# Kernel optimization log

Measured on AMD Instinct MI355X. Metric: run time of the kernel, lower is better.

The kernel has to match this reference:

```python
import jax, jax.numpy as jnp
import numpy as np

EPS = 1e-08
LAM = 0.01


def setup_inputs() -> dict:
    key = jax.random.key(0)
    k1, k2, k3 = jax.random.split(key, 3)
    BS, L, N = 256, 2048, 128
    pred_weights = jax.random.normal(k1, (BS, L, N), dtype=jnp.float32)
    # positive prices in [0.5, 1.5) to avoid div-by-zero / inf
    price_list = jax.random.uniform(k2, (BS, L + 1, N), dtype=jnp.float32, minval=0.5, maxval=1.5)
    # valid lengths in [2, L] (torch.var is unbiased -> need n >= 2)
    pred_sz = jax.random.randint(k3, (BS, 1), 2, L + 1, dtype=jnp.int64)
    return {"pred_weights": pred_weights, "price_list": price_list, "pred_sz": pred_sz}


def reference(pred_weights, price_list, pred_sz):
    P_i = price_list[:, :-1, :]  # [BS, L, N] past prices
    P_j = price_list[:, 1:, :]   # [BS, L, N] future prices
    r = jnp.nan_to_num((P_j - P_i) / P_i)
    r = r * (r <= 2)             # zero out returns > 2 (outlier mask)

    L = r.shape[1]
    Rp = jnp.sum(pred_weights[:, :L, :] * r, axis=-1)  # [BS, L] portfolio returns

    n = pred_sz.reshape(-1).astype(Rp.dtype)                       # [BS]
    mask = (jnp.arange(L)[None, :] < pred_sz.reshape(-1, 1)).astype(Rp.dtype)  # [BS, L]

    expected_Rp = jnp.sum(Rp * mask, axis=1) / n                   # masked mean
    centered = (Rp - expected_Rp[:, None]) * mask
    variance_Rp = jnp.sum(centered * centered, axis=1) / (n - 1)   # unbiased var (torch.var default)

    denom = jnp.sqrt(variance_Rp + EPS)
    sharpe = expected_Rp / denom
    sharpe_list = expected_Rp - LAM / denom

    return (-jnp.mean(sharpe_list), -jnp.mean(sharpe), jnp.mean(expected_Rp), jnp.mean(variance_Rp))
```

## Files before the change

### kernel.cpp

```cpp
#include <hip/hip_runtime.h>

#define EPS 1e-8f
#define LAM 0.01f

constexpr int BS = 256;
constexpr int L  = 2048;
constexpr int N  = 128;
constexpr int CHUNK  = 128;
constexpr int NCHUNK = L / CHUNK;


__global__ __launch_bounds__(256) void rp_kernel(
    const float* __restrict__ w,
    const float* __restrict__ price,
    const int*  __restrict__ pred_sz,
    float* __restrict__ ws)
{
    const int b     = blockIdx.x / NCHUNK;
    const int chunk = blockIdx.x % NCHUNK;
    const int n     = pred_sz[b];

    const int start = chunk * CHUNK;
    if (start >= n) return;
    const int end = min(start + CHUNK, n);

    const int tid  = threadIdx.x;
    const int grp  = tid >> 5;
    const int lane = tid & 31;

    float s1 = 0.0f, s2 = 0.0f;

    const int l0 = start + grp;
    const float* wp = w     + ((size_t)b * L       + l0) * N + lane * 4;
    const float* pp = price + ((size_t)b * (L + 1) + l0) * N + lane * 4;

    #pragma unroll 4
    for (int l = l0; l < end; l += 8, wp += 8 * N, pp += 8 * N) {
        const float4 wv = *reinterpret_cast<const float4*>(wp);
        const float4 pi = *reinterpret_cast<const float4*>(pp);
        const float4 pj = *reinterpret_cast<const float4*>(pp + N);

        float r0 = (pj.x - pi.x) * __builtin_amdgcn_rcpf(pi.x);
        float r1 = (pj.y - pi.y) * __builtin_amdgcn_rcpf(pi.y);
        float r2 = (pj.z - pi.z) * __builtin_amdgcn_rcpf(pi.z);
        float r3 = (pj.w - pi.w) * __builtin_amdgcn_rcpf(pi.w);
        r0 = (r0 <= 2.0f) ? r0 : 0.0f;
        r1 = (r1 <= 2.0f) ? r1 : 0.0f;
        r2 = (r2 <= 2.0f) ? r2 : 0.0f;
        r3 = (r3 <= 2.0f) ? r3 : 0.0f;

        float acc = wv.x * r0 + wv.y * r1 + wv.z * r2 + wv.w * r3;

        #pragma unroll
        for (int m = 1; m < 32; m <<= 1)
            acc += __shfl_xor(acc, m);

        if (lane == 0) {
            s1 += acc;
            s2 += acc * acc;
        }
    }

    __shared__ float ls1[8], ls2[8];
    if (lane == 0) { ls1[grp] = s1; ls2[grp] = s2; }
    __syncthreads();
    if (tid == 0) {
        float t1 = 0.0f, t2 = 0.0f;
        #pragma unroll
        for (int i = 0; i < 8; ++i) { t1 += ls1[i]; t2 += ls2[i]; }
        ws[b * NCHUNK + chunk]              = t1;
        ws[BS * NCHUNK + b * NCHUNK + chunk] = t2;
    }
}

__global__ __launch_bounds__(256) void final_kernel(
    const float* __restrict__ ws,
    const int*  __restrict__ pred_sz,
    float* __restrict__ out)
{
    const int b = threadIdx.x;
    const int ni = pred_sz[b];
    const int nc = (ni + CHUNK - 1) / CHUNK;

    float s1 = 0.0f, s2 = 0.0f;
    for (int c = 0; c < nc; ++c) {
        s1 += ws[b * NCHUNK + c];
        s2 += ws[BS * NCHUNK + b * NCHUNK + c];
    }

    const float n  = (float)ni;
    const float E     = s1 / n;
    const float var   = (s2 - n * E * E) / (n - 1.0f);
    const float denom = sqrtf(var + EPS);
    const float sharpe      = E / denom;
    const float sharpe_list = E - LAM / denom;

    __shared__ float red[4][BS];
    red[0][b] = sharpe_list;
    red[1][b] = sharpe;
    red[2][b] = E;
    red[3][b] = var;
    __syncthreads();

    #pragma unroll
    for (int s = BS / 2; s > 0; s >>= 1) {
        if (b < s) {
            red[0][b] += red[0][b + s];
            red[1][b] += red[1][b + s];
            red[2][b] += red[2][b + s];
            red[3][b] += red[3][b + s];
        }
        __syncthreads();
    }

    if (b == 0) {
        out[0] = -red[0][0] / (float)BS;
        out[1] = -red[1][0] / (float)BS;
        out[2] =  red[2][0] / (float)BS;
        out[3] =  red[3][0] / (float)BS;
    }
}

extern "C" void kernel_launch(void* const* d_in, const int* in_sizes, int n_in,
                              void* d_out, int out_size, void* d_ws, size_t ws_size,
                              hipStream_t stream) {
    const float* w     = (const float*)d_in[0];
    const float* price = (const float*)d_in[1];
    const int*   psz   = (const int*)d_in[2];
    float* out = (float*)d_out;
    float* ws  = (float*)d_ws;

    rp_kernel<<<BS * NCHUNK, 256, 0, stream>>>(w, price, psz, ws);
    final_kernel<<<1, BS, 0, stream>>>(ws, psz, out);
}
```

Measured before the change: 67.63 us.

## Process contiguous 16-row batches per group with price reuse and transposed shuffle reduction

Each 32-lane group now handles contiguous runs of 16 rows and reuses the previous row's price vector as the next row's past price, so price traffic is roughly halved. Instead of a full 5-step butterfly per row, it runs a transpose-style shuffle reduction that folds 16 row sums together, cutting shuffle count per row. CHUNK doubles to 256 so each block covers more rows and the grid halves. The cost is more registers for the 16-entry accumulator, which may lower occupancy.

```diff
diff --git a/kernel.cpp b/kernel.cpp
--- a/kernel.cpp
+++ b/kernel.cpp
@@ -6,7 +6,7 @@
 constexpr int BS = 256;
 constexpr int L  = 2048;
 constexpr int N  = 128;
-constexpr int CHUNK  = 128;
+constexpr int CHUNK  = 256;
 constexpr int NCHUNK = L / CHUNK;
 
 
@@ -30,37 +30,62 @@
 
     float s1 = 0.0f, s2 = 0.0f;
 
-    const int l0 = start + grp;
-    const float* wp = w     + ((size_t)b * L       + l0) * N + lane * 4;
-    const float* pp = price + ((size_t)b * (L + 1) + l0) * N + lane * 4;
+    #pragma unroll
+    for (int batch = 0; batch < 2; ++batch) {
+        const int rs = start + grp * 32 + batch * 16;
 
-    #pragma unroll 4
-    for (int l = l0; l < end; l += 8, wp += 8 * N, pp += 8 * N) {
-        const float4 wv = *reinterpret_cast<const float4*>(wp);
-        const float4 pi = *reinterpret_cast<const float4*>(pp);
-        const float4 pj = *reinterpret_cast<const float4*>(pp + N);
+        float A[16];
+        #pragma unroll
+        for (int r = 0; r < 16; ++r) A[r] = 0.0f;
 
-        float r0 = (pj.x - pi.x) * __builtin_amdgcn_rcpf(pi.x);
-        float r1 = (pj.y - pi.y) * __builtin_amdgcn_rcpf(pi.y);
-        float r2 = (pj.z - pi.z) * __builtin_amdgcn_rcpf(pi.z);
-        float r3 = (pj.w - pi.w) * __builtin_amdgcn_rcpf(pi.w);
-        r0 = (r0 <= 2.0f) ? r0 : 0.0f;
-        r1 = (r1 <= 2.0f) ? r1 : 0.0f;
-        r2 = (r2 <= 2.0f) ? r2 : 0.0f;
-        r3 = (r3 <= 2.0f) ? r3 : 0.0f;
+        if (rs < end) {
+            const float* wp = w     + ((size_t)b * L       + rs) * N + lane * 4;
+            const float* pp = price + ((size_t)b * (L + 1) + rs) * N + lane * 4;
 
-        float acc = wv.x * r0 + wv.y * r1 + wv.z * r2 + wv.w * r3;
+            float4 pv = *reinterpret_cast<const float4*>(pp);
+            #pragma unroll
+            for (int r = 0; r < 16; ++r) {
+                if (rs + r < end) {
+                    const float4 pj = *reinterpret_cast<const float4*>(pp + (size_t)(r + 1) * N);
+                    const float4 wv = *reinterpret_cast<const float4*>(wp + (size_t)r * N);
+
+                    float r0 = (pj.x - pv.x) * __builtin_amdgcn_rcpf(pv.x);
+                    float r1 = (pj.y - pv.y) * __builtin_amdgcn_rcpf(pv.y);
+                    float r2 = (pj.z - pv.z) * __builtin_amdgcn_rcpf(pv.z);
+                    float r3 = (pj.w - pv.w) * __builtin_amdgcn_rcpf(pv.w);
+                    r0 = (r0 <= 2.0f) ? r0 : 0.0f;
+                    r1 = (r1 <= 2.0f) ? r1 : 0.0f;
+                    r2 = (r2 <= 2.0f) ? r2 : 0.0f;
+                    r3 = (r3 <= 2.0f) ? r3 : 0.0f;
+
+                    A[r] = wv.x * r0 + wv.y * r1 + wv.z * r2 + wv.w * r3;
+                    pv = pj;
+                }
+            }
+        }
 
         #pragma unroll
-        for (int m = 1; m < 32; m <<= 1)
-            acc += __shfl_xor(acc, m);
-
-        if (lane == 0) {
-            s1 += acc;
-            s2 += acc * acc;
+        for (int k = 0; k < 4; ++k) {
+            const int  m  = 1 << k;
+            const bool hi = (lane & m) != 0;
+            #pragma unroll
+            for (int t = 0; t < (8 >> k); ++t) {
+                const float send = hi ? A[2 * t] : A[2 * t + 1];
+                const float recv = __shfl_xor(send, m);
+                A[t] = (hi ? A[2 * t + 1] : A[2 * t]) + recv;
+            }
         }
+        const float v = A[0] + __shfl_xor(A[0], 16);
+        const float vm = (lane & 16) ? 0.0f : v;
+        s1 += vm;
+        s2 += vm * vm;
     }
 
+    #pragma unroll
+    for (int m = 1; m < 32; m <<= 1) {
+        s1 += __shfl_xor(s1, m);
+        s2 += __shfl_xor(s2, m);
+    }
     __shared__ float ls1[8], ls2[8];
     if (lane == 0) { ls1[grp] = s1; ls2[grp] = s2; }
     __syncthreads();
@@ -68,7 +93,7 @@
         float t1 = 0.0f, t2 = 0.0f;
         #pragma unroll
         for (int i = 0; i < 8; ++i) { t1 += ls1[i]; t2 += ls2[i]; }
-        ws[b * NCHUNK + chunk]              = t1;
+        ws[b * NCHUNK + chunk]               = t1;
         ws[BS * NCHUNK + b * NCHUNK + chunk] = t2;
     }
 }
@@ -88,7 +113,7 @@
         s2 += ws[BS * NCHUNK + b * NCHUNK + c];
     }
 
-    const float n  = (float)ni;
+    const float n     = (float)ni;
     const float E     = s1 / n;
     const float var   = (s2 - n * E * E) / (n - 1.0f);
     const float denom = sqrtf(var + EPS);
```

Result: slower. 75.21 us (+11.2%).
